# Optimization experiments

Measured on AMD Instinct MI355X. Metric: run time of the kernel, lower is better.

## Reference

```python
import jax, jax.numpy as jnp
import numpy as np

EPS = 1e-5
CLUSTER_COUNT = 64
B, N, DV, DA = 128, 300, 1024, 128


def setup_inputs() -> dict:
    key = jax.random.key(0)
    k1, k2 = jax.random.split(key)
    video = jax.random.normal(k1, (B, N, DV), dtype=jnp.float32)
    audio = jax.random.normal(k2, (B, N, DA), dtype=jnp.float32)
    return {"video": video, "audio": audio}


def _select_indices(x_norm):
    """Greedy farthest-point (min |cosine|) selection for one batch. x_norm: [N, D]."""
    # indices starts as [0]; first appended index comes from sims of row 0
    best = jnp.abs(x_norm @ x_norm[0])          # [N]
    last = jnp.argmin(best)

    def step(carry, _):
        best, last = carry
        sims = jnp.abs(x_norm @ x_norm[last])   # [N]
        best = jnp.maximum(best, sims)
        new_last = jnp.argmin(best)
        return (best, new_last), new_last

    (_, _), rest = jax.lax.scan(step, (best, last), None, length=CLUSTER_COUNT - 2)
    idx = jnp.concatenate([jnp.array([0], dtype=last.dtype),
                           last[None], rest])  # [CLUSTER_COUNT]
    return jnp.sort(idx)


def reference(video, audio):
    # video: [B, N, DV], audio: [B, N, DA]
    norm = jnp.linalg.norm(video, axis=2) + EPS          # [B, N]
    video_normalized = video / norm[:, :, None]
    idx = jax.vmap(_select_indices)(video_normalized)     # [B, K], sorted
    v_sel = jnp.take_along_axis(video, idx[:, :, None], axis=1)  # [B, K, DV]
    a_sel = jnp.take_along_axis(audio, idx[:, :, None], axis=1)  # [B, K, DA]
    return v_sel, a_sel
```

## Files before the change

kernel.cpp:

```cpp
#include <hip/hip_runtime.h>
#include <math.h>


constexpr int BB = 128, NN = 300, DV = 1024, DA = 128, KK = 64;
constexpr int TRI = NN * (NN + 1) / 2;
constexpr int TB = 64;
constexpr int NTILES = 15;
constexpr int KC = 32;
constexpr int NCH = DV / KC;
constexpr int LDH = 36;

__device__ __constant__ int c_ib[NTILES] = {0,0,0,0,0, 1,1,1,1, 2,2,2, 3,3, 4};
__device__ __constant__ int c_jb[NTILES] = {0,1,2,3,4, 1,2,3,4, 2,3,4, 3,4, 4};

typedef _Float16 f16x8 __attribute__((ext_vector_type(8)));
typedef float    f32x4 __attribute__((ext_vector_type(4)));

union H4 { _Float16 h[4]; uint2 u; };
union F8 { uint2 u2[2]; f16x8 v; };

__device__ __forceinline__ int tri_base(int i) { return i * NN - (i * (i - 1)) / 2; }

__global__ __launch_bounds__(256) void kgram(const float* __restrict__ video,
                                             float* __restrict__ G) {
    const int bid  = blockIdx.x;
    const int swz  = (bid & 7) * 240 + (bid >> 3);
    const int batch = swz / 15;
    const int tile  = swz - batch * 15;
    const int i0 = c_ib[tile] * TB, j0 = c_jb[tile] * TB;
    const bool diag = (i0 == j0);
    const int tid = threadIdx.x;

    __shared__ _Float16 sH[2][4][TB][LDH];
    __shared__ float    s_part[256];
    __shared__ double   s_inv[2][TB];

    const float* vb = video + (size_t)batch * NN * DV;

    const int slab  = tid >> 7;
    const int lrow  = (tid >> 1) & 63;
    const int khalf = tid & 1;
    const int grow  = (slab ? j0 : i0) + lrow;
    const bool rok  = grow < NN;
    const bool stage_on = !(diag && slab == 1);
    const float4* srcb4 = (const float4*)(vb + (size_t)(rok ? grow : 0) * DV);
    const int qbase = khalf * 4;

    const int lane = tid & 63, w = tid >> 6;
    const int wr = w >> 1, wc = w & 1;
    const int g = lane >> 4, c16 = lane & 15;
    const int bplane = diag ? 0 : 2;

    f32x4 acc[2][2];
    #pragma unroll
    for (int fr = 0; fr < 2; ++fr)
        #pragma unroll
        for (int fc = 0; fc < 2; ++fc) acc[fr][fc] = (f32x4){0.f, 0.f, 0.f, 0.f};

    float ps = 0.f;
    float4 ld[4];
    const float4 z4 = make_float4(0.f, 0.f, 0.f, 0.f);

    auto stage_write = [&](int bf) {
        #pragma unroll
        for (int q = 0; q < 4; ++q) {
            float4 v = ld[q];
            ps = fmaf(v.x, v.x, fmaf(v.y, v.y, fmaf(v.z, v.z, fmaf(v.w, v.w, ps))));
            H4 hi, lo;
            _Float16 h0 = (_Float16)v.x, h1 = (_Float16)v.y,
                     h2 = (_Float16)v.z, h3 = (_Float16)v.w;
            hi.h[0] = h0; hi.h[1] = h1; hi.h[2] = h2; hi.h[3] = h3;
            lo.h[0] = (_Float16)(v.x - (float)h0);
            lo.h[1] = (_Float16)(v.y - (float)h1);
            lo.h[2] = (_Float16)(v.z - (float)h2);
            lo.h[3] = (_Float16)(v.w - (float)h3);
            const int p = khalf * 16 + 4 * q;
            *(uint2*)&sH[bf][slab * 2 + 0][lrow][p] = hi.u;
            *(uint2*)&sH[bf][slab * 2 + 1][lrow][p] = lo.u;
        }
    };

    if (stage_on) {
        #pragma unroll
        for (int q = 0; q < 4; ++q) ld[q] = rok ? srcb4[qbase + q] : z4;
        stage_write(0);
        #pragma unroll
        for (int q = 0; q < 4; ++q) ld[q] = rok ? srcb4[8 + qbase + q] : z4;
    }
    __syncthreads();

    for (int kc = 0; kc < NCH; ++kc) {
        const int cur = kc & 1, nxt = cur ^ 1;

        if (stage_on && kc < NCH - 1) stage_write(nxt);
        if (stage_on && kc < NCH - 2) {
            #pragma unroll
            for (int q = 0; q < 4; ++q)
                ld[q] = rok ? srcb4[(kc + 2) * 8 + qbase + q] : z4;
        }

        f16x8 Ah[2], Al[2], Bh[2], Bl[2];
        #pragma unroll
        for (int fr = 0; fr < 2; ++fr) {
            const int row = 32 * wr + 16 * fr + c16;
            F8 t;
            t.u2[0] = *(const uint2*)&sH[cur][0][row][4 * g];
            t.u2[1] = *(const uint2*)&sH[cur][0][row][16 + 4 * g];
            Ah[fr] = t.v;
            t.u2[0] = *(const uint2*)&sH[cur][1][row][4 * g];
            t.u2[1] = *(const uint2*)&sH[cur][1][row][16 + 4 * g];
            Al[fr] = t.v;
        }
        #pragma unroll
        for (int fc = 0; fc < 2; ++fc) {
            const int row = 32 * wc + 16 * fc + c16;
            F8 t;
            t.u2[0] = *(const uint2*)&sH[cur][bplane + 0][row][4 * g];
            t.u2[1] = *(const uint2*)&sH[cur][bplane + 0][row][16 + 4 * g];
            Bh[fc] = t.v;
            t.u2[0] = *(const uint2*)&sH[cur][bplane + 1][row][4 * g];
            t.u2[1] = *(const uint2*)&sH[cur][bplane + 1][row][16 + 4 * g];
            Bl[fc] = t.v;
        }
        #pragma unroll
        for (int fr = 0; fr < 2; ++fr)
            #pragma unroll
            for (int fc = 0; fc < 2; ++fc) {
                acc[fr][fc] = __builtin_amdgcn_mfma_f32_16x16x32_f16(Ah[fr], Bh[fc], acc[fr][fc], 0, 0, 0);
                acc[fr][fc] = __builtin_amdgcn_mfma_f32_16x16x32_f16(Ah[fr], Bl[fc], acc[fr][fc], 0, 0, 0);
                acc[fr][fc] = __builtin_amdgcn_mfma_f32_16x16x32_f16(Al[fr], Bh[fc], acc[fr][fc], 0, 0, 0);
            }

        __syncthreads();
    }

    s_part[tid] = ps;
    __syncthreads();
    if (tid < 128) {
        const int sl = tid >> 6, r = tid & 63;
        const int src = (sl && !diag) ? 128 + 2 * r : 2 * r;
        float ssum = s_part[src] + s_part[src + 1];
        s_inv[sl][r] = 1.0 / (sqrt((double)ssum) + 1e-5);
    }
    __syncthreads();

    float* Gb = G + (size_t)batch * TRI;
    #pragma unroll
    for (int fr = 0; fr < 2; ++fr)
        #pragma unroll
        for (int fc = 0; fc < 2; ++fc)
            #pragma unroll
            for (int reg = 0; reg < 4; ++reg) {
                const int il = 32 * wr + 16 * fr + 4 * g + reg;
                const int jl = 32 * wc + 16 * fc + c16;
                const int i = i0 + il, j = j0 + jl;
                if (i <= j && j < NN)
                    Gb[tri_base(i) + (j - i)] =
                        (float)(fabs((double)acc[fr][fc][reg]) * s_inv[0][il] * s_inv[1][jl]);
            }
}

__device__ __forceinline__ void select_wave_tri(const float* __restrict__ Gb,
                                                int lane, int* s_sorted) {
    float best[5];
    int myidx = 0;

    #pragma unroll
    for (int q = 0; q < 5; ++q) {
        int r = lane + 64 * q;
        best[q] = (r < NN) ? Gb[r] : 3.4e38f;
    }

    int last;
    {
        float v = INFINITY; int ri = 1 << 30;
        #pragma unroll
        for (int q = 0; q < 5; ++q)
            if (best[q] < v) { v = best[q]; ri = lane + 64 * q; }
        #pragma unroll
        for (int off = 32; off >= 1; off >>= 1) {
            float ov = __shfl_xor(v, off, 64); int oi = __shfl_xor(ri, off, 64);
            if (ov < v || (ov == v && oi < ri)) { v = ov; ri = oi; }
        }
        last = ri;
    }
    if (lane == 1) myidx = last;

    for (int t = 2; t < KK; ++t) {
        #pragma unroll
        for (int q = 0; q < 5; ++q) {
            int r = lane + 64 * q;
            if (r < NN) {
                int i = min(last, r), j = max(last, r);
                best[q] = fmaxf(best[q], Gb[tri_base(i) + (j - i)]);
            }
        }
        float v = INFINITY; int ri = 1 << 30;
        #pragma unroll
        for (int q = 0; q < 5; ++q)
            if (best[q] < v) { v = best[q]; ri = lane + 64 * q; }
        #pragma unroll
        for (int off = 32; off >= 1; off >>= 1) {
            float ov = __shfl_xor(v, off, 64); int oi = __shfl_xor(ri, off, 64);
            if (ov < v || (ov == v && oi < ri)) { v = ov; ri = oi; }
        }
        last = ri;
        if (lane == t) myidx = last;
    }

    int rank = 0;
    for (int j = 0; j < KK; ++j) {
        int oj = __shfl(myidx, j, 64);
        rank += (oj < myidx) || (oj == myidx && j < lane);
    }
    s_sorted[rank] = myidx;
}

__global__ __launch_bounds__(256) void kfused(const float* __restrict__ G,
                                              const float* __restrict__ video,
                                              const float* __restrict__ audio,
                                              float* __restrict__ out_v,
                                              float* __restrict__ out_a) {
    const int b = (blockIdx.x & 7) * 16 + (blockIdx.x >> 3);
    const int tid = threadIdx.x;
    __shared__ int s_sorted[KK];

    if (tid < 64)
        select_wave_tri(G + (size_t)b * TRI, tid, s_sorted);
    __syncthreads();

    const float4* vb4 = (const float4*)(video + (size_t)b * NN * DV);
    float4* ov4 = (float4*)(out_v + (size_t)b * KK * DV);
    #pragma unroll 4
    for (int t = tid; t < KK * DV / 4; t += 256) {
        int k = t >> 8, c = t & 255;
        ov4[t] = vb4[s_sorted[k] * (DV / 4) + c];
    }
    const float4* ab4 = (const float4*)(audio + (size_t)b * NN * DA);
    float4* oa4 = (float4*)(out_a + (size_t)b * KK * DA);
    for (int t = tid; t < KK * DA / 4; t += 256) {
        int k = t >> 5, c = t & 31;
        oa4[t] = ab4[s_sorted[k] * (DA / 4) + c];
    }
}

__global__ __launch_bounds__(64) void kselect(const float* __restrict__ G,
                                              float* __restrict__ out_a) {
    __shared__ int s_sorted[KK];
    select_wave_tri(G + (size_t)blockIdx.x * TRI, threadIdx.x, s_sorted);
    __syncthreads();
    ((int*)(out_a + (size_t)blockIdx.x * KK * DA))[threadIdx.x] = s_sorted[threadIdx.x];
}

__global__ __launch_bounds__(256) void kgather(const float* __restrict__ video,
                                               const float* __restrict__ audio,
                                               float* __restrict__ out_v,
                                               float* __restrict__ out_a) {
    int b = blockIdx.x, tid = threadIdx.x;
    __shared__ int s_idx[KK];
    const int* idxp = (const int*)(out_a + (size_t)b * KK * DA);
    if (tid < KK) s_idx[tid] = idxp[tid];
    __syncthreads();

    const float4* vb4 = (const float4*)(video + (size_t)b * NN * DV);
    float4* ov4 = (float4*)(out_v + (size_t)b * KK * DV);
    #pragma unroll 4
    for (int t = tid; t < KK * DV / 4; t += 256) {
        int k = t >> 8, c = t & 255;
        ov4[t] = vb4[s_idx[k] * (DV / 4) + c];
    }
    const float4* ab4 = (const float4*)(audio + (size_t)b * NN * DA);
    float4* oa4 = (float4*)(out_a + (size_t)b * KK * DA);
    for (int t = tid; t < KK * DA / 4; t += 256) {
        int k = t >> 5, c = t & 31;
        oa4[t] = ab4[s_idx[k] * (DA / 4) + c];
    }
}

extern "C" void kernel_launch(void* const* d_in, const int* in_sizes, int n_in,
                              void* d_out, int out_size, void* d_ws, size_t ws_size,
                              hipStream_t stream) {
    const float* video = (const float*)d_in[0];
    const float* audio = (const float*)d_in[1];
    float* out   = (float*)d_out;
    float* out_v = out;
    float* out_a = out + (size_t)BB * KK * DV;

    const size_t g_bytes = (size_t)BB * TRI * sizeof(float);

    if (ws_size >= g_bytes) {
        float* G = (float*)d_ws;
        kgram <<<NTILES * BB, 256, 0, stream>>>(video, G);
        kfused<<<BB, 256, 0, stream>>>(G, video, audio, out_v, out_a);
    } else {
        float* G = out;
        kgram  <<<NTILES * BB, 256, 0, stream>>>(video, G);
        kselect<<<BB, 64, 0, stream>>>(G, out_a);
        kgather<<<BB, 256, 0, stream>>>(video, audio, out_v, out_a);
    }
}
```

Before: 207.3 us.

## Fuse greedy selection into gram kernel via last-block atomic counter; split gather

Each gram tile block increments a per-batch atomic counter after writing its part of G. The last block to finish a batch runs the greedy farthest-point selection and writes the sorted indices to the workspace. The gather then runs as a separate kernel with four blocks per batch, so it uses more parallelism than the old one-block-per-batch fused select+gather. This overlaps the serial selection with remaining gram tiles, at the cost of an extra memset launch, atomics and fences.

Result: slower. 491.6 us (+137.2%).

```diff
diff --git a/kernel.cpp b/kernel.cpp
--- a/kernel.cpp
+++ b/kernel.cpp
@@ -10,6 +10,11 @@
 constexpr int NCH = DV / KC;
 constexpr int LDH = 36;
 
+constexpr size_t G_BYTES = (size_t)BB * TRI * 4;
+constexpr size_t CNT_OFF = G_BYTES;
+constexpr size_t IDX_OFF = CNT_OFF + 512;
+constexpr size_t WS_NEED = IDX_OFF + (size_t)BB * KK * 4;
+
 __device__ __constant__ int c_ib[NTILES] = {0,0,0,0,0, 1,1,1,1, 2,2,2, 3,3, 4};
 __device__ __constant__ int c_jb[NTILES] = {0,1,2,3,4, 1,2,3,4, 2,3,4, 3,4, 4};
 
@@ -21,8 +26,67 @@
 
 __device__ __forceinline__ int tri_base(int i) { return i * NN - (i * (i - 1)) / 2; }
 
+__device__ __forceinline__ void select_wave_tri(const float* __restrict__ Gb,
+                                                int lane, int* s_sorted) {
+    float best[5];
+    int myidx = 0;
+
+    #pragma unroll
+    for (int q = 0; q < 5; ++q) {
+        int r = lane + 64 * q;
+        best[q] = (r < NN) ? Gb[r] : 3.4e38f;
+    }
+
+    int last;
+    {
+        float v = INFINITY; int ri = 1 << 30;
+        #pragma unroll
+        for (int q = 0; q < 5; ++q)
+            if (best[q] < v) { v = best[q]; ri = lane + 64 * q; }
+        #pragma unroll
+        for (int off = 32; off >= 1; off >>= 1) {
+            float ov = __shfl_xor(v, off, 64); int oi = __shfl_xor(ri, off, 64);
+            if (ov < v || (ov == v && oi < ri)) { v = ov; ri = oi; }
+        }
+        last = ri;
+    }
+    if (lane == 1) myidx = last;
+
+    for (int t = 2; t < KK; ++t) {
+        #pragma unroll
+        for (int q = 0; q < 5; ++q) {
+            int r = lane + 64 * q;
+            if (r < NN) {
+                int i = min(last, r), j = max(last, r);
+                best[q] = fmaxf(best[q], Gb[tri_base(i) + (j - i)]);
+            }
+        }
+        float v = INFINITY; int ri = 1 << 30;
+        #pragma unroll
+        for (int q = 0; q < 5; ++q)
+            if (best[q] < v) { v = best[q]; ri = lane + 64 * q; }
+        #pragma unroll
+        for (int off = 32; off >= 1; off >>= 1) {
+            float ov = __shfl_xor(v, off, 64); int oi = __shfl_xor(ri, off, 64);
+            if (ov < v || (ov == v && oi < ri)) { v = ov; ri = oi; }
+        }
+        last = ri;
+        if (lane == t) myidx = last;
+    }
+
+    int rank = 0;
+    for (int j = 0; j < KK; ++j) {
+        int oj = __shfl(myidx, j, 64);
+        rank += (oj < myidx) || (oj == myidx && j < lane);
+    }
+    s_sorted[rank] = myidx;
+}
+
+template <bool DOSEL>
 __global__ __launch_bounds__(256) void kgram(const float* __restrict__ video,
-                                             float* __restrict__ G) {
+                                             float* __restrict__ G,
+                                             int* __restrict__ cnt,
+                                             int* __restrict__ idx) {
     const int bid  = blockIdx.x;
     const int swz  = (bid & 7) * 240 + (bid >> 3);
     const int batch = swz / 15;
@@ -34,6 +98,8 @@
     __shared__ _Float16 sH[2][4][TB][LDH];
     __shared__ float    s_part[256];
     __shared__ double   s_inv[2][TB];
+    __shared__ int      s_sorted[KK];
+    __shared__ int      s_flag;
 
     const float* vb = video + (size_t)batch * NN * DV;
 
@@ -158,89 +224,48 @@
                     Gb[tri_base(i) + (j - i)] =
                         (float)(fabs((double)acc[fr][fc][reg]) * s_inv[0][il] * s_inv[1][jl]);
             }
-}
-
-__device__ __forceinline__ void select_wave_tri(const float* __restrict__ Gb,
-                                                int lane, int* s_sorted) {
-    float best[5];
-    int myidx = 0;
-
-    #pragma unroll
-    for (int q = 0; q < 5; ++q) {
-        int r = lane + 64 * q;
-        best[q] = (r < NN) ? Gb[r] : 3.4e38f;
-    }
-
-    int last;
-    {
-        float v = INFINITY; int ri = 1 << 30;
-        #pragma unroll
-        for (int q = 0; q < 5; ++q)
-            if (best[q] < v) { v = best[q]; ri = lane + 64 * q; }
-        #pragma unroll
-        for (int off = 32; off >= 1; off >>= 1) {
-            float ov = __shfl_xor(v, off, 64); int oi = __shfl_xor(ri, off, 64);
-            if (ov < v || (ov == v && oi < ri)) { v = ov; ri = oi; }
-        }
-        last = ri;
-    }
-    if (lane == 1) myidx = last;
-
-    for (int t = 2; t < KK; ++t) {
-        #pragma unroll
-        for (int q = 0; q < 5; ++q) {
-            int r = lane + 64 * q;
-            if (r < NN) {
-                int i = min(last, r), j = max(last, r);
-                best[q] = fmaxf(best[q], Gb[tri_base(i) + (j - i)]);
-            }
-        }
-        float v = INFINITY; int ri = 1 << 30;
-        #pragma unroll
-        for (int q = 0; q < 5; ++q)
-            if (best[q] < v) { v = best[q]; ri = lane + 64 * q; }
-        #pragma unroll
-        for (int off = 32; off >= 1; off >>= 1) {
-            float ov = __shfl_xor(v, off, 64); int oi = __shfl_xor(ri, off, 64);
-            if (ov < v || (ov == v && oi < ri)) { v = ov; ri = oi; }
-        }
-        last = ri;
-        if (lane == t) myidx = last;
-    }
-
-    int rank = 0;
-    for (int j = 0; j < KK; ++j) {
-        int oj = __shfl(myidx, j, 64);
-        rank += (oj < myidx) || (oj == myidx && j < lane);
-    }
-    s_sorted[rank] = myidx;
-}
-
-__global__ __launch_bounds__(256) void kfused(const float* __restrict__ G,
-                                              const float* __restrict__ video,
-                                              const float* __restrict__ audio,
-                                              float* __restrict__ out_v,
-                                              float* __restrict__ out_a) {
-    const int b = (blockIdx.x & 7) * 16 + (blockIdx.x >> 3);
-    const int tid = threadIdx.x;
-    __shared__ int s_sorted[KK];
-
-    if (tid < 64)
-        select_wave_tri(G + (size_t)b * TRI, tid, s_sorted);
+
+    if (DOSEL) {
+        __threadfence();
+        __syncthreads();
+        if (tid == 0)
+            s_flag = (atomicAdd(&cnt[batch], 1) == NTILES - 1);
+        __syncthreads();
+        if (s_flag) {
+            __threadfence();
+            if (tid < 64)
+                select_wave_tri(Gb, tid, s_sorted);
+            __syncthreads();
+            if (tid < KK)
+                idx[batch * KK + tid] = s_sorted[tid];
+        }
+    }
+}
+
+__global__ __launch_bounds__(256) void kgath(const int* __restrict__ idx,
+                                             const float* __restrict__ video,
+                                             const float* __restrict__ audio,
+                                             float* __restrict__ out_v,
+                                             float* __restrict__ out_a) {
+    const int b = blockIdx.x >> 2, quar = blockIdx.x & 3, tid = threadIdx.x;
+    __shared__ int s_idx[KK];
+    if (tid < KK) s_idx[tid] = idx[b * KK + tid];
     __syncthreads();
 
     const float4* vb4 = (const float4*)(video + (size_t)b * NN * DV);
     float4* ov4 = (float4*)(out_v + (size_t)b * KK * DV);
+    const int vbeg = quar * 4096, vend = vbeg + 4096;
     #pragma unroll 4
-    for (int t = tid; t < KK * DV / 4; t += 256) {
+    for (int t = vbeg + tid; t < vend; t += 256) {
         int k = t >> 8, c = t & 255;
-        ov4[t] = vb4[s_sorted[k] * (DV / 4) + c];
+        ov4[t] = vb4[s_idx[k] * (DV / 4) + c];
     }
     const float4* ab4 = (const float4*)(audio + (size_t)b * NN * DA);
     float4* oa4 = (float4*)(out_a + (size_t)b * KK * DA);
-    for (int t = tid; t < KK * DA / 4; t += 256) {
+    const int abeg = quar * 512, aend = abeg + 512;
+    for (int t = abeg + tid; t < aend; t += 256) {
         int k = t >> 5, c = t & 31;
-        oa4[t] = ab4[s_sorted[k] * (DA / 4) + c];
+        oa4[t] = ab4[s_idx[k] * (DA / 4) + c];
     }
 }
 
@@ -286,15 +311,16 @@
     float* out_v = out;
     float* out_a = out + (size_t)BB * KK * DV;
 
-    const size_t g_bytes = (size_t)BB * TRI * sizeof(float);
-
-    if (ws_size >= g_bytes) {
+    if (ws_size >= WS_NEED) {
         float* G = (float*)d_ws;
-        kgram <<<NTILES * BB, 256, 0, stream>>>(video, G);
-        kfused<<<BB, 256, 0, stream>>>(G, video, audio, out_v, out_a);
+        int* cnt = (int*)((char*)d_ws + CNT_OFF);
+        int* idx = (int*)((char*)d_ws + IDX_OFF);
+        hipMemsetAsync(cnt, 0, 512, stream);
+        kgram<true><<<NTILES * BB, 256, 0, stream>>>(video, G, cnt, idx);
+        kgath<<<4 * BB, 256, 0, stream>>>(idx, video, audio, out_v, out_a);
     } else {
         float* G = out;
-        kgram  <<<NTILES * BB, 256, 0, stream>>>(video, G);
+        kgram<false><<<NTILES * BB, 256, 0, stream>>>(video, G, nullptr, nullptr);
         kselect<<<BB, 64, 0, stream>>>(G, out_a);
         kgather<<<BB, 256, 0, stream>>>(video, audio, out_v, out_a);
     }
```
